# Kernel optimization log

Measured on AMD Instinct MI355X. Metric: run time of the kernel, lower is better.

## Reference

```python
import jax, jax.numpy as jnp
import numpy as np

DIM = 1024
HEADS = 16
HEAD_DIM = DIM // HEADS
SCALE = HEAD_DIM ** -0.5


def setup_inputs() -> dict:
    key = jax.random.key(0)
    k_x, k_win, k_wout, k_bout = jax.random.split(key, 4)
    x = jax.random.normal(k_x, (4, 2048, DIM), dtype=jnp.float32)
    # torch Linear: y = x @ W.T + b; store weights as [in, out] for jnp
    w_in = jax.random.normal(k_win, (DIM, 3 * DIM), dtype=jnp.float32) * (DIM ** -0.5)
    w_out = jax.random.normal(k_wout, (DIM, DIM), dtype=jnp.float32) * (DIM ** -0.5)
    b_out = jax.random.normal(k_bout, (DIM,), dtype=jnp.float32) * 0.02
    return {"x": x, "w_in": w_in, "w_out": w_out, "b_out": b_out}


def reference(x, w_in, w_out, b_out):
    b, n, _ = x.shape
    qkv = x @ w_in  # [b, n, 3*dim]
    q, k, v = jnp.split(qkv, 3, axis=-1)
    # [b, n, h*d] -> [b, h, n, d]
    def split_heads(t):
        return t.reshape(b, n, HEADS, HEAD_DIM).transpose(0, 2, 1, 3)
    q, k, v = split_heads(q), split_heads(k), split_heads(v)
    scores = jnp.einsum('bhid,bhjd->bhij', q, k) * SCALE
    attn = jax.nn.softmax(scores, axis=-1)  # dropout_rate=0 -> identity
    o = jnp.einsum('bhij,bhjd->bhid', attn, v)
    o = o.transpose(0, 2, 1, 3).reshape(b, n, HEADS * HEAD_DIM)
    return o @ w_out + b_out
```

## Files before the change

### kernel.cpp

```cpp
#include <hip/hip_runtime.h>

typedef unsigned short u16;
typedef __bf16 bf16x8 __attribute__((ext_vector_type(8)));
typedef float f32x4 __attribute__((ext_vector_type(4)));
typedef unsigned short u16x4 __attribute__((ext_vector_type(4)));
typedef unsigned short u16x8 __attribute__((ext_vector_type(8)));

#define DIM 1024
#define HEADS 16
#define HD 64
#define SEQ 2048
#define BATCH 4
#define NROWS (BATCH*SEQ)
#define C2 0.18033688f
#define DEFER_THR 30.0f

__device__ __forceinline__ u16 f2bf(float f) {
  union { float f; unsigned u; } v; v.f = f;
  unsigned r = v.u + 0x7FFFu + ((v.u >> 16) & 1u);
  return (u16)(r >> 16);
}

__device__ __forceinline__ unsigned cvt_pk_bf16(float lo, float hi) {
  unsigned r;
  asm("v_cvt_pk_bf16_f32 %0, %1, %2" : "=v"(r) : "v"(lo), "v"(hi));
  return r;
}

__device__ __forceinline__ f32x4 mfma16(bf16x8 a, bf16x8 b, f32x4 c) {
  return __builtin_amdgcn_mfma_f32_16x16x32_bf16(a, b, c, 0, 0, 0);
}

__device__ __forceinline__ void gl_lds16(const void* g, void* l) {
  __builtin_amdgcn_global_load_lds(
      (const __attribute__((address_space(1))) void*)g,
      (__attribute__((address_space(3))) void*)l, 16, 0, 0);
}

__global__ __launch_bounds__(256) void cast_f32_bf16(const float* __restrict__ in,
                                                     u16* __restrict__ out) {
  int i = blockIdx.x * 256 + threadIdx.x;
  float4 v = ((const float4*)in)[i];
  u16x4 o = { f2bf(v.x), f2bf(v.y), f2bf(v.z), f2bf(v.w) };
  *(u16x4*)(out + (size_t)i * 4) = o;
}

__global__ __launch_bounds__(256) void transpose_cast(const float* __restrict__ in,
                                                      u16* __restrict__ out,
                                                      int R, int C) {
  __shared__ u16 tile[64][65];
  int c0 = blockIdx.x * 64, r0 = blockIdx.y * 64;
  int tid = threadIdx.x;
#pragma unroll
  for (int i = 0; i < 16; ++i) {
    int idx = tid + i * 256;
    int r = idx >> 6, c = idx & 63;
    tile[c][r] = f2bf(in[(size_t)(r0 + r) * C + c0 + c]);
  }
  __syncthreads();
#pragma unroll
  for (int i = 0; i < 16; ++i) {
    int idx = tid + i * 256;
    int r = idx >> 6, c = idx & 63;
    out[(size_t)(c0 + r) * R + r0 + c] = tile[r][c];
  }
}

__global__ __launch_bounds__(256) void transpose_v(const u16* __restrict__ qkv,
                                                   u16* __restrict__ vT) {
  __shared__ unsigned t32[64][37];
  const int t = blockIdx.x, bh = blockIdx.y;
  const int b = bh >> 4, h = bh & 15;
  const u16* src = qkv + ((size_t)(b * SEQ + t * 64)) * 3072 + 2048 + h * 64;
  const int tid = threadIdx.x;
#pragma unroll
  for (int i = 0; i < 8; ++i) {
    int lin = tid + i * 256;
    int r2 = lin >> 6, c = lin & 63;
    unsigned lo = src[(size_t)(2 * r2) * 3072 + c];
    unsigned hi = src[(size_t)(2 * r2 + 1) * 3072 + c];
    t32[c][r2] = lo | (hi << 16);
  }
  __syncthreads();
  unsigned* dst = (unsigned*)(vT + (size_t)bh * 64 * 2048);
#pragma unroll
  for (int i = 0; i < 8; ++i) {
    int lin = tid + i * 256;
    int d = lin >> 5, r2 = lin & 31;
    dst[(size_t)d * 1024 + t * 32 + r2] = t32[d][r2];
  }
}

template<int OUT_F32>
__global__ __launch_bounds__(256) void gemm_bt(const u16* __restrict__ A,
                                               const u16* __restrict__ BT,
                                               void* __restrict__ Cout,
                                               const float* __restrict__ bias,
                                               int M, int N, int K) {
  __shared__ __align__(16) u16 As[128 * 64];
  __shared__ __align__(16) u16 Bs[128 * 64];
  const int tid = threadIdx.x;
  const int l = tid & 63, w = tid >> 6, g = l >> 4, ln = l & 15;
  const int m0 = blockIdx.y * 128, n0 = blockIdx.x * 128;
  const int wr = w >> 1, wc = w & 1;
  f32x4 acc[4][4];
#pragma unroll
  for (int i = 0; i < 4; ++i)
#pragma unroll
    for (int j = 0; j < 4; ++j) acc[i][j] = (f32x4){0.f, 0.f, 0.f, 0.f};

  const int srow = tid >> 3;
  const int scol = (tid & 7) * 8;
  const u16* Asrc = A  + (size_t)(m0 + srow) * K + scol;
  const u16* Bsrc = BT + (size_t)(n0 + srow) * K + scol;
  char* AsB = (char*)As + (size_t)w * 1024;
  char* BsB = (char*)Bs + (size_t)w * 1024;

  const int nk = K >> 6;
  for (int kt = 0; kt < nk; ++kt) {
    const u16* a0 = Asrc + kt * 64;
    const u16* b0 = Bsrc + kt * 64;
#pragma unroll
    for (int is = 0; is < 4; ++is) {
      gl_lds16(a0 + (size_t)is * 32 * K, AsB + is * 4096);
      gl_lds16(b0 + (size_t)is * 32 * K, BsB + is * 4096);
    }
    __syncthreads();
#pragma unroll
    for (int kk = 0; kk < 2; ++kk) {
      bf16x8 af[4], bfr[4];
#pragma unroll
      for (int i = 0; i < 4; ++i) {
        af[i]  = *(const bf16x8*)(As + (wr * 64 + i * 16 + ln) * 64 + kk * 32 + g * 8);
        bfr[i] = *(const bf16x8*)(Bs + (wc * 64 + i * 16 + ln) * 64 + kk * 32 + g * 8);
      }
#pragma unroll
      for (int mi = 0; mi < 4; ++mi)
#pragma unroll
        for (int ni = 0; ni < 4; ++ni)
          acc[mi][ni] = mfma16(af[mi], bfr[ni], acc[mi][ni]);
    }
    __syncthreads();
  }
#pragma unroll
  for (int mi = 0; mi < 4; ++mi) {
#pragma unroll
    for (int ni = 0; ni < 4; ++ni) {
      int col = n0 + wc * 64 + ni * 16 + ln;
#pragma unroll
      for (int j = 0; j < 4; ++j) {
        int row = m0 + wr * 64 + mi * 16 + g * 4 + j;
        float v = acc[mi][ni][j];
        if (OUT_F32) {
          ((float*)Cout)[(size_t)row * N + col] = v + bias[col];
        } else {
          ((u16*)Cout)[(size_t)row * N + col] = f2bf(v);
        }
      }
    }
  }
}

__global__ __launch_bounds__(256) void attn_kernel(const u16* __restrict__ qkv,
                                                   const u16* __restrict__ vT,
                                                   u16* __restrict__ obuf) {
  __shared__ __align__(16) u16 k_lds[64 * 64];
  __shared__ __align__(16) u16 v_lds[64 * 64];
  const int wg = blockIdx.x;
  const int j = (wg & 7) * 256 + (wg >> 3);
  const int qt = j & 31, h = (j >> 5) & 15, b = j >> 9;
  const int tid = threadIdx.x;
  const int w = tid >> 6, l = tid & 63, g = l >> 4, ln = l & 15;
  const int qrow = qt * 64 + w * 16 + ln;
  const size_t rs = 3 * DIM;
  const u16* qb = qkv + (size_t)(b * SEQ + qrow) * rs + h * HD;
  bf16x8 qf0 = *(const bf16x8*)(qb + g * 8);
  bf16x8 qf1 = *(const bf16x8*)(qb + 32 + g * 8);

  const int krow = tid >> 3;
  const int ksrccol = ((((tid & 7) << 4) ^ ((krow & 7) << 4))) >> 1;
  const u16* kbase = qkv + (size_t)b * SEQ * rs + DIM + h * HD;
  const u16* vtb = vT + (size_t)(b * HEADS + h) * 64 * 2048;
  char* kdst = (char*)k_lds + (size_t)w * 1024;
  char* vdst = (char*)v_lds + (size_t)w * 1024;

  const int swz = (ln & 7) << 4;

  float m = -1e30f, lsum = 0.f;
  f32x4 of[4];
#pragma unroll
  for (int i = 0; i < 4; ++i) of[i] = (f32x4){0.f, 0.f, 0.f, 0.f};

  for (int kv0 = 0; kv0 < SEQ; kv0 += 64) {
    const u16* ks0 = kbase + (size_t)(kv0 + krow) * rs + ksrccol;
    const u16* vs0 = vtb + (size_t)krow * 2048 + kv0 + ksrccol;
    gl_lds16(ks0, kdst);
    gl_lds16(ks0 + (size_t)32 * rs, kdst + 4096);
    gl_lds16(vs0, vdst);
    gl_lds16(vs0 + (size_t)32 * 2048, vdst + 4096);
    __syncthreads();

    f32x4 sacc[4];
#pragma unroll
    for (int f = 0; f < 4; ++f) sacc[f] = (f32x4){0.f, 0.f, 0.f, 0.f};
#pragma unroll
    for (int f = 0; f < 4; ++f) {
      const char* kr = (const char*)k_lds + (f * 16 + ln) * 128;
      bf16x8 a0 = *(const bf16x8*)(kr + ((g * 16) ^ swz));
      bf16x8 a1 = *(const bf16x8*)(kr + ((64 | (g * 16)) ^ swz));
      sacc[f] = mfma16(a0, qf0, sacc[f]);
      sacc[f] = mfma16(a1, qf1, sacc[f]);
    }

    float tm = -3e38f;
#pragma unroll
    for (int f = 0; f < 4; ++f)
#pragma unroll
      for (int jj = 0; jj < 4; ++jj) tm = fmaxf(tm, sacc[f][jj]);
    tm = fmaxf(tm, __shfl_xor(tm, 16));
    tm = fmaxf(tm, __shfl_xor(tm, 32));
    if (__any(tm > m + DEFER_THR)) {
      float mn = fmaxf(m, tm);
      float rs2 = __builtin_amdgcn_exp2f((m - mn) * C2);
      lsum *= rs2;
#pragma unroll
      for (int fd = 0; fd < 4; ++fd) of[fd] *= rs2;
      m = mn;
    }
    const float mc = m * C2;
    float ps = 0.f;
    union pu { unsigned wd[4]; bf16x8 b; } pf[2];
#pragma unroll
    for (int f = 0; f < 4; ++f) {
#pragma unroll
      for (int j2 = 0; j2 < 2; ++j2) {
        float p0 = __builtin_amdgcn_exp2f(fmaf(sacc[f][2 * j2], C2, -mc));
        float p1 = __builtin_amdgcn_exp2f(fmaf(sacc[f][2 * j2 + 1], C2, -mc));
        ps += p0 + p1;
        pf[f >> 1].wd[(f & 1) * 2 + j2] = cvt_pk_bf16(p0, p1);
      }
    }
    ps += __shfl_xor(ps, 16);
    ps += __shfl_xor(ps, 32);
    lsum += ps;

#pragma unroll
    for (int kk = 0; kk < 2; ++kk) {
#pragma unroll
      for (int fd = 0; fd < 4; ++fd) {
        const char* vr = (const char*)v_lds + (fd * 16 + ln) * 128;
        union { bf16x8 b; struct { u16x4 lo, hi; } hv; } fa;
        fa.hv.lo = *(const u16x4*)(vr + ((64 * kk + 8 * g) ^ swz));
        fa.hv.hi = *(const u16x4*)(vr + ((64 * kk + 32 + 8 * g) ^ swz));
        of[fd] = mfma16(fa.b, pf[kk].b, of[fd]);
      }
    }
    __syncthreads();
  }

  float linv = 1.f / lsum;
  u16* orow = obuf + (size_t)(b * SEQ + qrow) * DIM + h * HD;
#pragma unroll
  for (int fd = 0; fd < 4; ++fd) {
    unsigned w0 = cvt_pk_bf16(of[fd][0] * linv, of[fd][1] * linv);
    unsigned w1 = cvt_pk_bf16(of[fd][2] * linv, of[fd][3] * linv);
    unsigned* dst = (unsigned*)(orow + fd * 16 + g * 4);
    dst[0] = w0;
    dst[1] = w1;
  }
}

extern "C" void kernel_launch(void* const* d_in, const int* in_sizes, int n_in,
                              void* d_out, int out_size, void* d_ws, size_t ws_size,
                              hipStream_t stream) {
  const float* x     = (const float*)d_in[0];
  const float* w_in  = (const float*)d_in[1];
  const float* w_out = (const float*)d_in[2];
  const float* b_out = (const float*)d_in[3];
  float* out = (float*)d_out;

  char* ws = (char*)d_ws;
  u16* xb     = (u16*)(ws);
  u16* vT     = (u16*)(ws);
  u16* w_inT  = (u16*)(ws + (size_t)16 * 1024 * 1024);
  u16* w_outT = (u16*)(ws + (size_t)22 * 1024 * 1024);
  u16* qkv    = (u16*)(ws + (size_t)24 * 1024 * 1024);
  u16* obuf   = (u16*)(ws + (size_t)72 * 1024 * 1024);

  cast_f32_bf16<<<8192, 256, 0, stream>>>(x, xb);
  transpose_cast<<<dim3(48, 16), 256, 0, stream>>>(w_in, w_inT, 1024, 3072);
  transpose_cast<<<dim3(16, 16), 256, 0, stream>>>(w_out, w_outT, 1024, 1024);
  gemm_bt<0><<<dim3(24, 64), 256, 0, stream>>>(xb, w_inT, qkv, nullptr, NROWS, 3 * DIM, DIM);
  transpose_v<<<dim3(32, 64), 256, 0, stream>>>(qkv, vT);
  attn_kernel<<<2048, 256, 0, stream>>>(qkv, vT, obuf);
  gemm_bt<1><<<dim3(8, 64), 256, 0, stream>>>(obuf, w_outT, out, b_out, NROWS, DIM, DIM);
}
```

Before: 255.3 us.

## Process two query sub-tiles per wave and defer softmax rescaling

Each attention wave now handles 32 query rows as two 16-row sub-tiles, so every K and V fragment read from LDS feeds twice as many MFMAs. The grid is halved to 1024 workgroups of 128 queries. The running-max check now runs only when the exp-sum overflows a large threshold, and the max reduction and rescale are skipped otherwise. The V transpose stores a permuted column order so each PV operand becomes a single 16-byte LDS load. The cost is higher register pressure, fewer workgroups in flight, and reliance on fp32 range when rescaling is skipped.

After: 230.8 us. 1.11x faster.

```diff
diff --git a/kernel.cpp b/kernel.cpp
--- a/kernel.cpp
+++ b/kernel.cpp
@@ -13,7 +13,7 @@
 #define BATCH 4
 #define NROWS (BATCH*SEQ)
 #define C2 0.18033688f
-#define DEFER_THR 30.0f
+#define THR_PS 1.125899907e15f
 
 __device__ __forceinline__ u16 f2bf(float f) {
   union { float f; unsigned u; } v; v.f = f;
@@ -87,7 +87,8 @@
   for (int i = 0; i < 8; ++i) {
     int lin = tid + i * 256;
     int d = lin >> 5, r2 = lin & 31;
-    dst[(size_t)d * 1024 + t * 32 + r2] = t32[d][r2];
+    int rp = (r2 & 16) | ((r2 & 6) << 1) | ((r2 & 8) >> 2) | (r2 & 1);
+    dst[(size_t)d * 1024 + t * 32 + rp] = t32[d][r2];
   }
 }
 
@@ -167,15 +168,20 @@
   __shared__ __align__(16) u16 k_lds[64 * 64];
   __shared__ __align__(16) u16 v_lds[64 * 64];
   const int wg = blockIdx.x;
-  const int j = (wg & 7) * 256 + (wg >> 3);
-  const int qt = j & 31, h = (j >> 5) & 15, b = j >> 9;
+  const int j = (wg & 7) * 128 + (wg >> 3);
+  const int qt = j & 15, h = (j >> 4) & 15, b = j >> 8;
   const int tid = threadIdx.x;
   const int w = tid >> 6, l = tid & 63, g = l >> 4, ln = l & 15;
-  const int qrow = qt * 64 + w * 16 + ln;
+  const int qbase = qt * 128 + w * 32;
   const size_t rs = 3 * DIM;
-  const u16* qb = qkv + (size_t)(b * SEQ + qrow) * rs + h * HD;
-  bf16x8 qf0 = *(const bf16x8*)(qb + g * 8);
-  bf16x8 qf1 = *(const bf16x8*)(qb + 32 + g * 8);
+
+  bf16x8 qf[2][2];
+#pragma unroll
+  for (int e = 0; e < 2; ++e) {
+    const u16* qb = qkv + (size_t)(b * SEQ + qbase + e * 16 + ln) * rs + h * HD;
+    qf[e][0] = *(const bf16x8*)(qb + g * 8);
+    qf[e][1] = *(const bf16x8*)(qb + 32 + g * 8);
+  }
 
   const int krow = tid >> 3;
   const int ksrccol = ((((tid & 7) << 4) ^ ((krow & 7) << 4))) >> 1;
@@ -183,13 +189,14 @@
   const u16* vtb = vT + (size_t)(b * HEADS + h) * 64 * 2048;
   char* kdst = (char*)k_lds + (size_t)w * 1024;
   char* vdst = (char*)v_lds + (size_t)w * 1024;
-
   const int swz = (ln & 7) << 4;
 
-  float m = -1e30f, lsum = 0.f;
-  f32x4 of[4];
-#pragma unroll
-  for (int i = 0; i < 4; ++i) of[i] = (f32x4){0.f, 0.f, 0.f, 0.f};
+  float m[2] = { -1e30f, -1e30f }, lsum[2] = { 0.f, 0.f };
+  f32x4 of[2][4];
+#pragma unroll
+  for (int e = 0; e < 2; ++e)
+#pragma unroll
+    for (int i = 0; i < 4; ++i) of[e][i] = (f32x4){0.f, 0.f, 0.f, 0.f};
 
   for (int kv0 = 0; kv0 < SEQ; kv0 += 64) {
     const u16* ks0 = kbase + (size_t)(kv0 + krow) * rs + ksrccol;
@@ -200,73 +207,102 @@
     gl_lds16(vs0 + (size_t)32 * 2048, vdst + 4096);
     __syncthreads();
 
-    f32x4 sacc[4];
-#pragma unroll
-    for (int f = 0; f < 4; ++f) sacc[f] = (f32x4){0.f, 0.f, 0.f, 0.f};
+    f32x4 sacc[2][4];
+#pragma unroll
+    for (int e = 0; e < 2; ++e)
+#pragma unroll
+      for (int f = 0; f < 4; ++f) sacc[e][f] = (f32x4){0.f, 0.f, 0.f, 0.f};
 #pragma unroll
     for (int f = 0; f < 4; ++f) {
       const char* kr = (const char*)k_lds + (f * 16 + ln) * 128;
       bf16x8 a0 = *(const bf16x8*)(kr + ((g * 16) ^ swz));
       bf16x8 a1 = *(const bf16x8*)(kr + ((64 | (g * 16)) ^ swz));
-      sacc[f] = mfma16(a0, qf0, sacc[f]);
-      sacc[f] = mfma16(a1, qf1, sacc[f]);
-    }
-
-    float tm = -3e38f;
-#pragma unroll
-    for (int f = 0; f < 4; ++f)
-#pragma unroll
-      for (int jj = 0; jj < 4; ++jj) tm = fmaxf(tm, sacc[f][jj]);
-    tm = fmaxf(tm, __shfl_xor(tm, 16));
-    tm = fmaxf(tm, __shfl_xor(tm, 32));
-    if (__any(tm > m + DEFER_THR)) {
-      float mn = fmaxf(m, tm);
-      float rs2 = __builtin_amdgcn_exp2f((m - mn) * C2);
-      lsum *= rs2;
-#pragma unroll
-      for (int fd = 0; fd < 4; ++fd) of[fd] *= rs2;
-      m = mn;
-    }
-    const float mc = m * C2;
-    float ps = 0.f;
-    union pu { unsigned wd[4]; bf16x8 b; } pf[2];
-#pragma unroll
-    for (int f = 0; f < 4; ++f) {
-#pragma unroll
-      for (int j2 = 0; j2 < 2; ++j2) {
-        float p0 = __builtin_amdgcn_exp2f(fmaf(sacc[f][2 * j2], C2, -mc));
-        float p1 = __builtin_amdgcn_exp2f(fmaf(sacc[f][2 * j2 + 1], C2, -mc));
-        ps += p0 + p1;
-        pf[f >> 1].wd[(f & 1) * 2 + j2] = cvt_pk_bf16(p0, p1);
-      }
-    }
-    ps += __shfl_xor(ps, 16);
-    ps += __shfl_xor(ps, 32);
-    lsum += ps;
-
-#pragma unroll
-    for (int kk = 0; kk < 2; ++kk) {
+#pragma unroll
+      for (int e = 0; e < 2; ++e) {
+        sacc[e][f] = mfma16(a0, qf[e][0], sacc[e][f]);
+        sacc[e][f] = mfma16(a1, qf[e][1], sacc[e][f]);
+      }
+    }
+
+    union pu { unsigned wd[4]; bf16x8 bv; } pf[2][2];
+    float ps[2];
+#pragma unroll
+    for (int e = 0; e < 2; ++e) {
+      const float mc = m[e] * C2;
+      float s2 = 0.f;
+#pragma unroll
+      for (int f = 0; f < 4; ++f)
+#pragma unroll
+        for (int j2 = 0; j2 < 2; ++j2) {
+          float p0 = __builtin_amdgcn_exp2f(fmaf(sacc[e][f][2 * j2], C2, -mc));
+          float p1 = __builtin_amdgcn_exp2f(fmaf(sacc[e][f][2 * j2 + 1], C2, -mc));
+          s2 += p0 + p1;
+          pf[e][f >> 1].wd[(f & 1) * 2 + j2] = cvt_pk_bf16(p0, p1);
+        }
+      s2 += __shfl_xor(s2, 16);
+      s2 += __shfl_xor(s2, 32);
+      ps[e] = s2;
+    }
+    if (__any(fmaxf(ps[0], ps[1]) > THR_PS)) {
+#pragma unroll
+      for (int e = 0; e < 2; ++e) {
+        float tm = -3e38f;
+#pragma unroll
+        for (int f = 0; f < 4; ++f)
+#pragma unroll
+          for (int jj = 0; jj < 4; ++jj) tm = fmaxf(tm, sacc[e][f][jj]);
+        tm = fmaxf(tm, __shfl_xor(tm, 16));
+        tm = fmaxf(tm, __shfl_xor(tm, 32));
+        float mn = fmaxf(m[e], tm);
+        float rc = __builtin_amdgcn_exp2f((m[e] - mn) * C2);
+        lsum[e] *= rc;
+#pragma unroll
+        for (int fd = 0; fd < 4; ++fd) of[e][fd] *= rc;
+        m[e] = mn;
+        const float mc = mn * C2;
+        float s2 = 0.f;
+#pragma unroll
+        for (int f = 0; f < 4; ++f)
+#pragma unroll
+          for (int j2 = 0; j2 < 2; ++j2) {
+            float p0 = __builtin_amdgcn_exp2f(fmaf(sacc[e][f][2 * j2], C2, -mc));
+            float p1 = __builtin_amdgcn_exp2f(fmaf(sacc[e][f][2 * j2 + 1], C2, -mc));
+            s2 += p0 + p1;
+            pf[e][f >> 1].wd[(f & 1) * 2 + j2] = cvt_pk_bf16(p0, p1);
+          }
+        s2 += __shfl_xor(s2, 16);
+        s2 += __shfl_xor(s2, 32);
+        ps[e] = s2;
+      }
+    }
+    lsum[0] += ps[0];
+    lsum[1] += ps[1];
+
+#pragma unroll
+    for (int kk = 0; kk < 2; ++kk)
 #pragma unroll
       for (int fd = 0; fd < 4; ++fd) {
         const char* vr = (const char*)v_lds + (fd * 16 + ln) * 128;
-        union { bf16x8 b; struct { u16x4 lo, hi; } hv; } fa;
-        fa.hv.lo = *(const u16x4*)(vr + ((64 * kk + 8 * g) ^ swz));
-        fa.hv.hi = *(const u16x4*)(vr + ((64 * kk + 32 + 8 * g) ^ swz));
-        of[fd] = mfma16(fa.b, pf[kk].b, of[fd]);
-      }
-    }
+        bf16x8 fa = *(const bf16x8*)(vr + ((kk * 64 + g * 16) ^ swz));
+#pragma unroll
+        for (int e = 0; e < 2; ++e)
+          of[e][fd] = mfma16(fa, pf[e][kk].bv, of[e][fd]);
+      }
     __syncthreads();
   }
 
-  float linv = 1.f / lsum;
-  u16* orow = obuf + (size_t)(b * SEQ + qrow) * DIM + h * HD;
-#pragma unroll
-  for (int fd = 0; fd < 4; ++fd) {
-    unsigned w0 = cvt_pk_bf16(of[fd][0] * linv, of[fd][1] * linv);
-    unsigned w1 = cvt_pk_bf16(of[fd][2] * linv, of[fd][3] * linv);
-    unsigned* dst = (unsigned*)(orow + fd * 16 + g * 4);
-    dst[0] = w0;
-    dst[1] = w1;
+#pragma unroll
+  for (int e = 0; e < 2; ++e) {
+    float linv = 1.f / lsum[e];
+    u16* orow = obuf + (size_t)(b * SEQ + qbase + e * 16 + ln) * DIM + h * HD;
+#pragma unroll
+    for (int fd = 0; fd < 4; ++fd) {
+      unsigned w0 = cvt_pk_bf16(of[e][fd][0] * linv, of[e][fd][1] * linv);
+      unsigned w1 = cvt_pk_bf16(of[e][fd][2] * linv, of[e][fd][3] * linv);
+      unsigned* dst = (unsigned*)(orow + fd * 16 + g * 4);
+      dst[0] = w0;
+      dst[1] = w1;
+    }
   }
 }
 
@@ -292,6 +328,6 @@
   transpose_cast<<<dim3(16, 16), 256, 0, stream>>>(w_out, w_outT, 1024, 1024);
   gemm_bt<0><<<dim3(24, 64), 256, 0, stream>>>(xb, w_inT, qkv, nullptr, NROWS, 3 * DIM, DIM);
   transpose_v<<<dim3(32, 64), 256, 0, stream>>>(qkv, vT);
-  attn_kernel<<<2048, 256, 0, stream>>>(qkv, vT, obuf);
+  attn_kernel<<<1024, 256, 0, stream>>>(qkv, vT, obuf);
   gemm_bt<1><<<dim3(8, 64), 256, 0, stream>>>(obuf, w_outT, out, b_out, NROWS, DIM, DIM);
 }
```
